# Performance work log

Measured on AMD Instinct MI355X. Metric: run time of the kernel, lower is better.

## Reference

```python
import jax, jax.numpy as jnp
import numpy as np

N_NODES = 50000
N_EDGES = 600000
F_IN, HID, N_CLS = 128, 128, 40
NEG_SLOPE = 0.2


def _gat_conv(x, src, dst, W, a_src, a_dst, b, num_nodes):
    # x: [N, Fin] -> h: [N, H]  (heads=1 PyG GATConv)
    h = x @ W
    s_src = h @ a_src  # [N]
    s_dst = h @ a_dst  # [N]
    e = jax.nn.leaky_relu(s_src[src] + s_dst[dst], NEG_SLOPE)  # [E]
    # numerically-stable softmax over incoming edges per destination node
    m = jax.ops.segment_max(e, dst, num_segments=num_nodes)  # [N]
    ex = jnp.exp(e - m[dst])
    denom = jax.ops.segment_sum(ex, dst, num_segments=num_nodes)  # [N]
    alpha = ex / denom[dst]  # [E]
    out = jax.ops.segment_sum(alpha[:, None] * h[src], dst, num_segments=num_nodes)
    return out + b


def setup_inputs() -> dict:
    key = jax.random.key(0)
    ks = jax.random.split(key, 10)
    x = jax.random.normal(ks[0], (N_NODES, F_IN), dtype=jnp.float32)
    edge_index = jax.random.randint(ks[1], (2, N_EDGES), 0, N_NODES, dtype=jnp.int64)
    sd = lambda fin: 1.0 / np.sqrt(fin)
    return {
        "x": x,
        "edge_index": edge_index,
        "W1": jax.random.normal(ks[2], (F_IN, HID), dtype=jnp.float32) * sd(F_IN),
        "a1_src": jax.random.normal(ks[3], (HID,), dtype=jnp.float32) * sd(HID),
        "a1_dst": jax.random.normal(ks[4], (HID,), dtype=jnp.float32) * sd(HID),
        "b1": jnp.zeros((HID,), dtype=jnp.float32),
        "W2": jax.random.normal(ks[5], (HID, HID), dtype=jnp.float32) * sd(HID),
        "a2_src": jax.random.normal(ks[6], (HID,), dtype=jnp.float32) * sd(HID),
        "a2_dst": jax.random.normal(ks[7], (HID,), dtype=jnp.float32) * sd(HID),
        "b2": jnp.zeros((HID,), dtype=jnp.float32),
        "Wl": jax.random.normal(ks[8], (HID, N_CLS), dtype=jnp.float32) * sd(HID),
        "bl": jnp.zeros((N_CLS,), dtype=jnp.float32),
    }


def reference(x, edge_index, W1, a1_src, a1_dst, b1, W2, a2_src, a2_dst, b2, Wl, bl):
    n = x.shape[0]
    # PyG GATConv adds self loops by default
    loops = jnp.arange(n, dtype=edge_index.dtype)
    src = jnp.concatenate([edge_index[0], loops])
    dst = jnp.concatenate([edge_index[1], loops])
    h = jax.nn.relu(_gat_conv(x, src, dst, W1, a1_src, a1_dst, b1, n))
    # F.dropout(training=self.training): eval mode -> identity
    h = _gat_conv(h, src, dst, W2, a2_src, a2_dst, b2, n)
    logits = jax.nn.log_softmax(h @ Wl + bl, axis=1)
    return (logits, edge_index)
```

## Files before the change

### kernel.cpp

```cpp
#include <hip/hip_runtime.h>
#include <hip/hip_bf16.h>
#include <math.h>

#define N_NODES 50000
#define N_EDGES 600000
#define TOT_E   (N_EDGES + N_NODES)
#define FDIM    128
#define HROW    64
#define NCLS    40
#define SCAN_B  1024

typedef __attribute__((ext_vector_type(4))) float  f32x4;
typedef __attribute__((ext_vector_type(8))) __bf16 bf16x8;
union FragU { uint32_t u[4]; bf16x8 v; };

__device__ inline float bf16_lo(uint32_t u) { return __uint_as_float(u << 16); }
__device__ inline float bf16_hi(uint32_t u) { return __uint_as_float(u & 0xffff0000u); }
__device__ inline uint32_t bf16_pack(float a, float b) {
    uint32_t ua = __float_as_uint(a), ub = __float_as_uint(b);
    uint32_t ra = (ua + 0x7fffu + ((ua >> 16) & 1u)) >> 16;
    uint32_t rb = (ub + 0x7fffu + ((ub >> 16) & 1u)) >> 16;
    return ra | (rb << 16);
}

#define PACK_BLOCKS 12500
__global__ __launch_bounds__(256) void setup_kernel(
        const float* __restrict__ x, uint32_t* __restrict__ Xp,
        const float* __restrict__ W1, const float* __restrict__ W2,
        uint32_t* __restrict__ wf1, uint32_t* __restrict__ wf2) {
    int b = blockIdx.x;
    if (b < PACK_BLOCKS) {
        int i = b * 256 + threadIdx.x;
        float2 v = ((const float2*)x)[i];
        Xp[i] = bf16_pack(v.x, v.y);
        return;
    }
    int t = (b - PACK_BLOCKS) * 256 + threadIdx.x;
    if (t >= 4096) return;
    const float* W = (t < 2048) ? W1 : W2;
    uint32_t*   wf = (t < 2048) ? wf1 : wf2;
    int q = t & 2047;
    int lane = q & 63, nt = (q >> 6) & 7, kt = q >> 9;
    int n = nt * 16 + (lane & 15), g = lane >> 4;
    uint32_t frag[4];
    #pragma unroll
    for (int d = 0; d < 4; d++) {
        int kb = kt * 32 + 4 * g + (d & 1) * 2 + (d >> 1) * 16;
        frag[d] = bf16_pack(W[kb * FDIM + n], W[(kb + 1) * FDIM + n]);
    }
    ((uint4*)wf)[(kt * 8 + nt) * 64 + lane] = *(uint4*)frag;
}

__global__ void hist_kernel(const int* __restrict__ ei, int* __restrict__ counts) {
    int i = blockIdx.x * blockDim.x + threadIdx.x;
    if (i >= N_EDGES / 4) return;
    int4 d = ((const int4*)(ei + N_EDGES))[i];
    atomicAdd(&counts[d.x], 1);
    atomicAdd(&counts[d.y], 1);
    atomicAdd(&counts[d.z], 1);
    atomicAdd(&counts[d.w], 1);
}

__global__ void scan1_kernel(const int* __restrict__ counts, int* __restrict__ excl,
                             int* __restrict__ bsums, int n) {
    __shared__ int ws[16];
    int gid = blockIdx.x * SCAN_B + threadIdx.x;
    int wv = threadIdx.x >> 6, lane = threadIdx.x & 63;
    int v = (gid < n) ? (counts[gid] + 1) : 0;
    int incl = v;
    #pragma unroll
    for (int off = 1; off < 64; off <<= 1) {
        int t = __shfl_up(incl, off, 64);
        if (lane >= off) incl += t;
    }
    if (lane == 63) ws[wv] = incl;
    __syncthreads();
    int woff = 0;
    for (int i = 0; i < wv; i++) woff += ws[i];
    if (gid < n) excl[gid] = woff + incl - v;
    if (threadIdx.x == SCAN_B - 1) bsums[blockIdx.x] = woff + incl;
}

__global__ void scan3_kernel(int* __restrict__ rowptr, const int* __restrict__ bsums,
                             int* __restrict__ cursor, int n, int total) {
    __shared__ int base_s;
    if (threadIdx.x < 64) {
        int v = (threadIdx.x < (int)blockIdx.x) ? bsums[threadIdx.x] : 0;
        #pragma unroll
        for (int off = 32; off > 0; off >>= 1) v += __shfl_down(v, off, 64);
        if (threadIdx.x == 0) base_s = v;
    }
    __syncthreads();
    int base = base_s;
    int gid = blockIdx.x * SCAN_B + threadIdx.x;
    if (gid < n) {
        int v = rowptr[gid] + base;
        rowptr[gid] = v;
        cursor[gid] = v;
    }
    if (gid == 0) rowptr[n] = total;
}

#define SCAT_T ((N_EDGES / 4) + N_NODES)
__global__ void scatter_kernel(const int* __restrict__ ei, int* __restrict__ cursor,
                               int* __restrict__ adj) {
    int i = blockIdx.x * blockDim.x + threadIdx.x;
    if (i >= SCAT_T) return;
    if (i < N_EDGES / 4) {
        int4 s4 = ((const int4*)ei)[i];
        int4 d4 = ((const int4*)(ei + N_EDGES))[i];
        adj[atomicAdd(&cursor[d4.x], 1)] = s4.x;
        adj[atomicAdd(&cursor[d4.y], 1)] = s4.y;
        adj[atomicAdd(&cursor[d4.z], 1)] = s4.z;
        adj[atomicAdd(&cursor[d4.w], 1)] = s4.w;
    } else {
        int nd = i - N_EDGES / 4;
        adj[atomicAdd(&cursor[nd], 1)] = nd;
    }
}

__global__ __launch_bounds__(256) void mfma_gemm(
        const uint32_t* __restrict__ Xp, const uint32_t* __restrict__ wf,
        const float* __restrict__ a_s, const float* __restrict__ a_d,
        uint32_t* __restrict__ H, float* __restrict__ ssrc, float* __restrict__ sdst) {
    int lane = threadIdx.x & 63, wv = threadIdx.x >> 6;
    int row0 = blockIdx.x * 64 + wv * 16;
    if (row0 >= N_NODES) return;
    int r = lane & 15, g = lane >> 4;

    const uint32_t* xrow = Xp + (size_t)(row0 + r) * HROW + 2 * g;
    FragU af[4];
    #pragma unroll
    for (int kt = 0; kt < 4; kt++) {
        uint2 lo = *(const uint2*)(xrow + kt * 16);
        uint2 hi = *(const uint2*)(xrow + kt * 16 + 8);
        af[kt].u[0] = lo.x; af[kt].u[1] = lo.y;
        af[kt].u[2] = hi.x; af[kt].u[3] = hi.y;
    }

    f32x4 acc[8] = {};
    #pragma unroll
    for (int kt = 0; kt < 4; kt++) {
        #pragma unroll
        for (int nt = 0; nt < 8; nt++) {
            FragU bfr;
            *(uint4*)bfr.u = ((const uint4*)wf)[(kt * 8 + nt) * 64 + lane];
            acc[nt] = __builtin_amdgcn_mfma_f32_16x16x32_bf16(af[kt].v, bfr.v, acc[nt], 0, 0, 0);
        }
    }

    float av_s[8], av_d[8];
    #pragma unroll
    for (int nt = 0; nt < 8; nt++) { av_s[nt] = a_s[16 * nt + r]; av_d[nt] = a_d[16 * nt + r]; }
    #pragma unroll
    for (int j = 0; j < 4; j++) {
        float ps = 0.f, pd = 0.f;
        #pragma unroll
        for (int nt = 0; nt < 8; nt++) { ps += acc[nt][j] * av_s[nt]; pd += acc[nt][j] * av_d[nt]; }
        #pragma unroll
        for (int off = 1; off < 16; off <<= 1) {
            ps += __shfl_xor(ps, off, 64);
            pd += __shfl_xor(pd, off, 64);
        }
        if (r == 0) { ssrc[row0 + 4 * g + j] = ps; sdst[row0 + 4 * g + j] = pd; }
    }

    #pragma unroll
    for (int nt = 0; nt < 8; nt++) {
        #pragma unroll
        for (int j = 0; j < 4; j++) {
            float v0 = acc[nt][j];
            float v1 = __shfl_xor(v0, 1, 64);
            if (!(r & 1)) {
                uint32_t p = bf16_pack(v0, v1);
                H[(size_t)(row0 + 4 * g + j) * HROW + nt * 8 + (r >> 1)] = p;
            }
        }
    }
}

__global__ __launch_bounds__(128) void gat_aggregate(
        const uint32_t* __restrict__ h, const float* __restrict__ ssrc,
        const float* __restrict__ sdst, const int* __restrict__ rowptr,
        const int* __restrict__ adj, const float* __restrict__ bias,
        uint32_t* __restrict__ out, int do_relu) {
    int wv = threadIdx.x >> 6, lane = threadIdx.x & 63;
    int sub = lane >> 4, l16 = lane & 15;
    int n = blockIdx.x * 2 + wv;
    __shared__ __align__(16) float wbuf[2][64];
    __shared__ __align__(16) int   sbuf[2][64];

    int beg = rowptr[n], deg = rowptr[n + 1] - beg;
    float sd = sdst[n];
    const uint4* h4 = (const uint4*)h;

    float acc[8] = {};
    float dsum = 0.f;

    for (int base = 0; base < deg; base += 64) {
        int c = min(64, deg - base);
        if (lane < c) {
            int s = adj[beg + base + lane];
            float e = ssrc[s] + sd;
            e = (e >= 0.f) ? e : 0.2f * e;
            float w = __expf(e);
            wbuf[wv][lane] = w;
            sbuf[wv][lane] = s;
            dsum += w;
        }
        asm volatile("s_waitcnt lgkmcnt(0)" ::: "memory");

        int j = 0;
        for (; j + 16 <= c; j += 16) {
            float4 w4 = *(const float4*)&wbuf[wv][j + 4 * sub];
            int4   s4 = *(const int4*)&sbuf[wv][j + 4 * sub];
            uint4 u0 = h4[(size_t)s4.x * 16 + l16];
            uint4 u1 = h4[(size_t)s4.y * 16 + l16];
            uint4 u2 = h4[(size_t)s4.z * 16 + l16];
            uint4 u3 = h4[(size_t)s4.w * 16 + l16];
            acc[0] += w4.x * bf16_lo(u0.x) + w4.y * bf16_lo(u1.x) + w4.z * bf16_lo(u2.x) + w4.w * bf16_lo(u3.x);
            acc[1] += w4.x * bf16_hi(u0.x) + w4.y * bf16_hi(u1.x) + w4.z * bf16_hi(u2.x) + w4.w * bf16_hi(u3.x);
            acc[2] += w4.x * bf16_lo(u0.y) + w4.y * bf16_lo(u1.y) + w4.z * bf16_lo(u2.y) + w4.w * bf16_lo(u3.y);
            acc[3] += w4.x * bf16_hi(u0.y) + w4.y * bf16_hi(u1.y) + w4.z * bf16_hi(u2.y) + w4.w * bf16_hi(u3.y);
            acc[4] += w4.x * bf16_lo(u0.z) + w4.y * bf16_lo(u1.z) + w4.z * bf16_lo(u2.z) + w4.w * bf16_lo(u3.z);
            acc[5] += w4.x * bf16_hi(u0.z) + w4.y * bf16_hi(u1.z) + w4.z * bf16_hi(u2.z) + w4.w * bf16_hi(u3.z);
            acc[6] += w4.x * bf16_lo(u0.w) + w4.y * bf16_lo(u1.w) + w4.z * bf16_lo(u2.w) + w4.w * bf16_lo(u3.w);
            acc[7] += w4.x * bf16_hi(u0.w) + w4.y * bf16_hi(u1.w) + w4.z * bf16_hi(u2.w) + w4.w * bf16_hi(u3.w);
        }
        for (; j < c; j += 4) {
            int e = j + sub;
            if (e < c) {
                float w = wbuf[wv][e];
                int   s = sbuf[wv][e];
                uint4 u = h4[(size_t)s * 16 + l16];
                acc[0] += w * bf16_lo(u.x); acc[1] += w * bf16_hi(u.x);
                acc[2] += w * bf16_lo(u.y); acc[3] += w * bf16_hi(u.y);
                acc[4] += w * bf16_lo(u.z); acc[5] += w * bf16_hi(u.z);
                acc[6] += w * bf16_lo(u.w); acc[7] += w * bf16_hi(u.w);
            }
        }
        asm volatile("" ::: "memory");
    }

    #pragma unroll
    for (int k = 0; k < 8; k++) {
        acc[k] += __shfl_xor(acc[k], 16, 64);
        acc[k] += __shfl_xor(acc[k], 32, 64);
    }
    #pragma unroll
    for (int off = 32; off > 0; off >>= 1) dsum += __shfl_xor(dsum, off, 64);

    if (sub == 0) {
        float inv = 1.f / dsum;
        float4 b0 = *(const float4*)&bias[l16 * 8];
        float4 b1 = *(const float4*)&bias[l16 * 8 + 4];
        float v0 = acc[0] * inv + b0.x, v1 = acc[1] * inv + b0.y;
        float v2 = acc[2] * inv + b0.z, v3 = acc[3] * inv + b0.w;
        float v4 = acc[4] * inv + b1.x, v5 = acc[5] * inv + b1.y;
        float v6 = acc[6] * inv + b1.z, v7 = acc[7] * inv + b1.w;
        if (do_relu) {
            v0 = fmaxf(v0, 0.f); v1 = fmaxf(v1, 0.f); v2 = fmaxf(v2, 0.f); v3 = fmaxf(v3, 0.f);
            v4 = fmaxf(v4, 0.f); v5 = fmaxf(v5, 0.f); v6 = fmaxf(v6, 0.f); v7 = fmaxf(v7, 0.f);
        }
        uint4 o;
        o.x = bf16_pack(v0, v1); o.y = bf16_pack(v2, v3);
        o.z = bf16_pack(v4, v5); o.w = bf16_pack(v6, v7);
        ((uint4*)out)[(size_t)n * 16 + l16] = o;
    }
}

#define CLS_BLOCKS  (N_NODES / 16)
#define EDGE_ITEMS  ((2 * N_EDGES) / 4)
#define EDGE_BLOCKS ((EDGE_ITEMS + 127) / 128)
__global__ __launch_bounds__(128) void classifier_edge_kernel(
        const uint32_t* __restrict__ H, const float* __restrict__ Wl,
        const float* __restrict__ bl, const int* __restrict__ ei,
        float* __restrict__ out, float* __restrict__ eout) {
    if (blockIdx.x >= CLS_BLOCKS) {
        int i = (blockIdx.x - CLS_BLOCKS) * 128 + threadIdx.x;
        if (i < EDGE_ITEMS) {
            int4 v = ((const int4*)ei)[i];
            ((float4*)eout)[i] = make_float4((float)v.x, (float)v.y, (float)v.z, (float)v.w);
        }
        return;
    }
    __shared__ float xs[16][FDIM];
    int tid  = threadIdx.x;
    int row0 = blockIdx.x * 16;
    const uint32_t* Hp = H + (size_t)row0 * HROW;
    #pragma unroll
    for (int i = 0; i < 8; i++) {
        int idx = tid + 128 * i;
        uint32_t u = Hp[idx];
        int r = idx >> 6, cc = idx & 63;
        xs[r][2 * cc]     = bf16_lo(u);
        xs[r][2 * cc + 1] = bf16_hi(u);
    }
    __syncthreads();

    int c = tid & 63, hw = tid >> 6;
    float acc[8];
    float blc = (c < NCLS) ? bl[c] : 0.f;
    #pragma unroll
    for (int r = 0; r < 8; r++) acc[r] = blc;

    #pragma unroll 2
    for (int k = 0; k < FDIM; k += 4) {
        float w0 = 0.f, w1 = 0.f, w2 = 0.f, w3 = 0.f;
        if (c < NCLS) {
            w0 = Wl[(k + 0) * NCLS + c]; w1 = Wl[(k + 1) * NCLS + c];
            w2 = Wl[(k + 2) * NCLS + c]; w3 = Wl[(k + 3) * NCLS + c];
        }
        #pragma unroll
        for (int r = 0; r < 8; r++) {
            float4 xv = *(const float4*)&xs[hw * 8 + r][k];
            acc[r] += xv.x * w0 + xv.y * w1 + xv.z * w2 + xv.w * w3;
        }
    }
    #pragma unroll
    for (int r = 0; r < 8; r++) {
        float v = (c < NCLS) ? acc[r] : -INFINITY;
        float mx = v;
        #pragma unroll
        for (int off = 32; off > 0; off >>= 1) mx = fmaxf(mx, __shfl_xor(mx, off, 64));
        float ex = (c < NCLS) ? expf(v - mx) : 0.f;
        #pragma unroll
        for (int off = 32; off > 0; off >>= 1) ex += __shfl_xor(ex, off, 64);
        float ls = logf(ex);
        if (c < NCLS) out[(size_t)(row0 + hw * 8 + r) * NCLS + c] = v - mx - ls;
    }
}

extern "C" void kernel_launch(void* const* d_in, const int* in_sizes, int n_in,
                              void* d_out, int out_size, void* d_ws, size_t ws_size,
                              hipStream_t stream) {
    const float* x   = (const float*)d_in[0];
    const int*   ei  = (const int*)d_in[1];
    const float* W1  = (const float*)d_in[2];
    const float* a1s = (const float*)d_in[3];
    const float* a1d = (const float*)d_in[4];
    const float* b1  = (const float*)d_in[5];
    const float* W2  = (const float*)d_in[6];
    const float* a2s = (const float*)d_in[7];
    const float* a2d = (const float*)d_in[8];
    const float* b2  = (const float*)d_in[9];
    const float* Wl  = (const float*)d_in[10];
    const float* bl  = (const float*)d_in[11];
    float* out = (float*)d_out;

    char* ws = (char*)d_ws;
    size_t off = 0;
    auto alloc = [&](size_t bytes) {
        void* p = ws + off;
        off = (off + bytes + 255) & ~(size_t)255;
        return p;
    };
    int*      row_ptr = (int*)alloc((N_NODES + 1) * sizeof(int));
    int*      cursor  = (int*)alloc(N_NODES * sizeof(int));
    int*      counts  = (int*)alloc(N_NODES * sizeof(int));
    int*      bsums   = (int*)alloc(64 * sizeof(int));
    int*      adj     = (int*)alloc(TOT_E * sizeof(int));
    uint32_t* Xp      = (uint32_t*)alloc((size_t)N_NODES * HROW * sizeof(uint32_t));
    uint32_t* hA      = (uint32_t*)alloc((size_t)N_NODES * HROW * sizeof(uint32_t));
    uint32_t* hB      = (uint32_t*)alloc((size_t)N_NODES * HROW * sizeof(uint32_t));
    float*    ssrc    = (float*)alloc(N_NODES * sizeof(float));
    float*    sdst    = (float*)alloc(N_NODES * sizeof(float));
    uint32_t* wf1     = (uint32_t*)alloc(2048 * 4 * sizeof(uint32_t));
    uint32_t* wf2     = (uint32_t*)alloc(2048 * 4 * sizeof(uint32_t));
    uint32_t* hC      = Xp;

    hipMemsetAsync(counts, 0, N_NODES * sizeof(int), stream);
    hipLaunchKernelGGL(setup_kernel, dim3(PACK_BLOCKS + 16), dim3(256), 0, stream,
                       x, Xp, W1, W2, wf1, wf2);

    hipLaunchKernelGGL(hist_kernel, dim3((N_EDGES / 4 + 255) / 256), dim3(256), 0, stream, ei, counts);
    int nscan = (N_NODES + SCAN_B - 1) / SCAN_B;
    hipLaunchKernelGGL(scan1_kernel, dim3(nscan), dim3(SCAN_B), 0, stream, counts, row_ptr, bsums, N_NODES);
    hipLaunchKernelGGL(scan3_kernel, dim3(nscan), dim3(SCAN_B), 0, stream, row_ptr, bsums, cursor, N_NODES, TOT_E);
    hipLaunchKernelGGL(scatter_kernel, dim3((SCAT_T + 255) / 256), dim3(256), 0, stream, ei, cursor, adj);

    hipLaunchKernelGGL(mfma_gemm, dim3((N_NODES + 63) / 64), dim3(256), 0, stream,
                       Xp, wf1, a1s, a1d, hA, ssrc, sdst);
    hipLaunchKernelGGL(gat_aggregate, dim3(N_NODES / 2), dim3(128), 0, stream,
                       hA, ssrc, sdst, row_ptr, adj, b1, hB, 1);

    hipLaunchKernelGGL(mfma_gemm, dim3((N_NODES + 63) / 64), dim3(256), 0, stream,
                       hB, wf2, a2s, a2d, hA, ssrc, sdst);
    hipLaunchKernelGGL(gat_aggregate, dim3(N_NODES / 2), dim3(128), 0, stream,
                       hA, ssrc, sdst, row_ptr, adj, b2, hC, 0);

    hipLaunchKernelGGL(classifier_edge_kernel, dim3(CLS_BLOCKS + EDGE_BLOCKS), dim3(128), 0, stream,
                       hC, Wl, bl, ei, out, out + (size_t)N_NODES * NCLS);
}
```

Baseline: 291.8 us.

## Fuse GAT pipeline into fewer kernels: agg+GEMM, agg+classifier, scatter+GEMM

```diff
diff --git a/kernel.cpp b/kernel.cpp
--- a/kernel.cpp
+++ b/kernel.cpp
@@ -23,180 +23,11 @@
     return ra | (rb << 16);
 }
 
-#define PACK_BLOCKS 12500
-__global__ __launch_bounds__(256) void setup_kernel(
-        const float* __restrict__ x, uint32_t* __restrict__ Xp,
-        const float* __restrict__ W1, const float* __restrict__ W2,
-        uint32_t* __restrict__ wf1, uint32_t* __restrict__ wf2) {
-    int b = blockIdx.x;
-    if (b < PACK_BLOCKS) {
-        int i = b * 256 + threadIdx.x;
-        float2 v = ((const float2*)x)[i];
-        Xp[i] = bf16_pack(v.x, v.y);
-        return;
-    }
-    int t = (b - PACK_BLOCKS) * 256 + threadIdx.x;
-    if (t >= 4096) return;
-    const float* W = (t < 2048) ? W1 : W2;
-    uint32_t*   wf = (t < 2048) ? wf1 : wf2;
-    int q = t & 2047;
-    int lane = q & 63, nt = (q >> 6) & 7, kt = q >> 9;
-    int n = nt * 16 + (lane & 15), g = lane >> 4;
-    uint32_t frag[4];
-    #pragma unroll
-    for (int d = 0; d < 4; d++) {
-        int kb = kt * 32 + 4 * g + (d & 1) * 2 + (d >> 1) * 16;
-        frag[d] = bf16_pack(W[kb * FDIM + n], W[(kb + 1) * FDIM + n]);
-    }
-    ((uint4*)wf)[(kt * 8 + nt) * 64 + lane] = *(uint4*)frag;
-}
-
-__global__ void hist_kernel(const int* __restrict__ ei, int* __restrict__ counts) {
-    int i = blockIdx.x * blockDim.x + threadIdx.x;
-    if (i >= N_EDGES / 4) return;
-    int4 d = ((const int4*)(ei + N_EDGES))[i];
-    atomicAdd(&counts[d.x], 1);
-    atomicAdd(&counts[d.y], 1);
-    atomicAdd(&counts[d.z], 1);
-    atomicAdd(&counts[d.w], 1);
-}
-
-__global__ void scan1_kernel(const int* __restrict__ counts, int* __restrict__ excl,
-                             int* __restrict__ bsums, int n) {
-    __shared__ int ws[16];
-    int gid = blockIdx.x * SCAN_B + threadIdx.x;
-    int wv = threadIdx.x >> 6, lane = threadIdx.x & 63;
-    int v = (gid < n) ? (counts[gid] + 1) : 0;
-    int incl = v;
-    #pragma unroll
-    for (int off = 1; off < 64; off <<= 1) {
-        int t = __shfl_up(incl, off, 64);
-        if (lane >= off) incl += t;
-    }
-    if (lane == 63) ws[wv] = incl;
-    __syncthreads();
-    int woff = 0;
-    for (int i = 0; i < wv; i++) woff += ws[i];
-    if (gid < n) excl[gid] = woff + incl - v;
-    if (threadIdx.x == SCAN_B - 1) bsums[blockIdx.x] = woff + incl;
-}
-
-__global__ void scan3_kernel(int* __restrict__ rowptr, const int* __restrict__ bsums,
-                             int* __restrict__ cursor, int n, int total) {
-    __shared__ int base_s;
-    if (threadIdx.x < 64) {
-        int v = (threadIdx.x < (int)blockIdx.x) ? bsums[threadIdx.x] : 0;
-        #pragma unroll
-        for (int off = 32; off > 0; off >>= 1) v += __shfl_down(v, off, 64);
-        if (threadIdx.x == 0) base_s = v;
-    }
-    __syncthreads();
-    int base = base_s;
-    int gid = blockIdx.x * SCAN_B + threadIdx.x;
-    if (gid < n) {
-        int v = rowptr[gid] + base;
-        rowptr[gid] = v;
-        cursor[gid] = v;
-    }
-    if (gid == 0) rowptr[n] = total;
-}
-
-#define SCAT_T ((N_EDGES / 4) + N_NODES)
-__global__ void scatter_kernel(const int* __restrict__ ei, int* __restrict__ cursor,
-                               int* __restrict__ adj) {
-    int i = blockIdx.x * blockDim.x + threadIdx.x;
-    if (i >= SCAT_T) return;
-    if (i < N_EDGES / 4) {
-        int4 s4 = ((const int4*)ei)[i];
-        int4 d4 = ((const int4*)(ei + N_EDGES))[i];
-        adj[atomicAdd(&cursor[d4.x], 1)] = s4.x;
-        adj[atomicAdd(&cursor[d4.y], 1)] = s4.y;
-        adj[atomicAdd(&cursor[d4.z], 1)] = s4.z;
-        adj[atomicAdd(&cursor[d4.w], 1)] = s4.w;
-    } else {
-        int nd = i - N_EDGES / 4;
-        adj[atomicAdd(&cursor[nd], 1)] = nd;
-    }
-}
-
-__global__ __launch_bounds__(256) void mfma_gemm(
-        const uint32_t* __restrict__ Xp, const uint32_t* __restrict__ wf,
-        const float* __restrict__ a_s, const float* __restrict__ a_d,
-        uint32_t* __restrict__ H, float* __restrict__ ssrc, float* __restrict__ sdst) {
-    int lane = threadIdx.x & 63, wv = threadIdx.x >> 6;
-    int row0 = blockIdx.x * 64 + wv * 16;
-    if (row0 >= N_NODES) return;
-    int r = lane & 15, g = lane >> 4;
-
-    const uint32_t* xrow = Xp + (size_t)(row0 + r) * HROW + 2 * g;
-    FragU af[4];
-    #pragma unroll
-    for (int kt = 0; kt < 4; kt++) {
-        uint2 lo = *(const uint2*)(xrow + kt * 16);
-        uint2 hi = *(const uint2*)(xrow + kt * 16 + 8);
-        af[kt].u[0] = lo.x; af[kt].u[1] = lo.y;
-        af[kt].u[2] = hi.x; af[kt].u[3] = hi.y;
-    }
-
-    f32x4 acc[8] = {};
-    #pragma unroll
-    for (int kt = 0; kt < 4; kt++) {
-        #pragma unroll
-        for (int nt = 0; nt < 8; nt++) {
-            FragU bfr;
-            *(uint4*)bfr.u = ((const uint4*)wf)[(kt * 8 + nt) * 64 + lane];
-            acc[nt] = __builtin_amdgcn_mfma_f32_16x16x32_bf16(af[kt].v, bfr.v, acc[nt], 0, 0, 0);
-        }
-    }
-
-    float av_s[8], av_d[8];
-    #pragma unroll
-    for (int nt = 0; nt < 8; nt++) { av_s[nt] = a_s[16 * nt + r]; av_d[nt] = a_d[16 * nt + r]; }
-    #pragma unroll
-    for (int j = 0; j < 4; j++) {
-        float ps = 0.f, pd = 0.f;
-        #pragma unroll
-        for (int nt = 0; nt < 8; nt++) { ps += acc[nt][j] * av_s[nt]; pd += acc[nt][j] * av_d[nt]; }
-        #pragma unroll
-        for (int off = 1; off < 16; off <<= 1) {
-            ps += __shfl_xor(ps, off, 64);
-            pd += __shfl_xor(pd, off, 64);
-        }
-        if (r == 0) { ssrc[row0 + 4 * g + j] = ps; sdst[row0 + 4 * g + j] = pd; }
-    }
-
-    #pragma unroll
-    for (int nt = 0; nt < 8; nt++) {
-        #pragma unroll
-        for (int j = 0; j < 4; j++) {
-            float v0 = acc[nt][j];
-            float v1 = __shfl_xor(v0, 1, 64);
-            if (!(r & 1)) {
-                uint32_t p = bf16_pack(v0, v1);
-                H[(size_t)(row0 + 4 * g + j) * HROW + nt * 8 + (r >> 1)] = p;
-            }
-        }
-    }
-}
-
-__global__ __launch_bounds__(128) void gat_aggregate(
-        const uint32_t* __restrict__ h, const float* __restrict__ ssrc,
-        const float* __restrict__ sdst, const int* __restrict__ rowptr,
-        const int* __restrict__ adj, const float* __restrict__ bias,
-        uint32_t* __restrict__ out, int do_relu) {
-    int wv = threadIdx.x >> 6, lane = threadIdx.x & 63;
-    int sub = lane >> 4, l16 = lane & 15;
-    int n = blockIdx.x * 2 + wv;
-    __shared__ __align__(16) float wbuf[2][64];
-    __shared__ __align__(16) int   sbuf[2][64];
-
-    int beg = rowptr[n], deg = rowptr[n + 1] - beg;
-    float sd = sdst[n];
-    const uint4* h4 = (const uint4*)h;
-
-    float acc[8] = {};
-    float dsum = 0.f;
-
+__device__ __forceinline__ void wave_agg_loop(
+        const uint4* __restrict__ h4, const float* __restrict__ ssrc,
+        const int* __restrict__ adj, float sd, int beg, int deg,
+        float* wb, int* sb, int lane, int sub, int l16,
+        float acc[8], float& dsum) {
     for (int base = 0; base < deg; base += 64) {
         int c = min(64, deg - base);
         if (lane < c) {
@@ -204,16 +35,16 @@
             float e = ssrc[s] + sd;
             e = (e >= 0.f) ? e : 0.2f * e;
             float w = __expf(e);
-            wbuf[wv][lane] = w;
-            sbuf[wv][lane] = s;
+            wb[lane] = w;
+            sb[lane] = s;
             dsum += w;
         }
         asm volatile("s_waitcnt lgkmcnt(0)" ::: "memory");
 
         int j = 0;
         for (; j + 16 <= c; j += 16) {
-            float4 w4 = *(const float4*)&wbuf[wv][j + 4 * sub];
-            int4   s4 = *(const int4*)&sbuf[wv][j + 4 * sub];
+            float4 w4 = *(const float4*)&wb[j + 4 * sub];
+            int4   s4 = *(const int4*)&sb[j + 4 * sub];
             uint4 u0 = h4[(size_t)s4.x * 16 + l16];
             uint4 u1 = h4[(size_t)s4.y * 16 + l16];
             uint4 u2 = h4[(size_t)s4.z * 16 + l16];
@@ -230,8 +61,8 @@
         for (; j < c; j += 4) {
             int e = j + sub;
             if (e < c) {
-                float w = wbuf[wv][e];
-                int   s = sbuf[wv][e];
+                float w = wb[e];
+                int   s = sb[e];
                 uint4 u = h4[(size_t)s * 16 + l16];
                 acc[0] += w * bf16_lo(u.x); acc[1] += w * bf16_hi(u.x);
                 acc[2] += w * bf16_lo(u.y); acc[3] += w * bf16_hi(u.y);
@@ -241,7 +72,6 @@
         }
         asm volatile("" ::: "memory");
     }
-
     #pragma unroll
     for (int k = 0; k < 8; k++) {
         acc[k] += __shfl_xor(acc[k], 16, 64);
@@ -249,60 +79,312 @@
     }
     #pragma unroll
     for (int off = 32; off > 0; off >>= 1) dsum += __shfl_xor(dsum, off, 64);
-
-    if (sub == 0) {
-        float inv = 1.f / dsum;
-        float4 b0 = *(const float4*)&bias[l16 * 8];
-        float4 b1 = *(const float4*)&bias[l16 * 8 + 4];
-        float v0 = acc[0] * inv + b0.x, v1 = acc[1] * inv + b0.y;
-        float v2 = acc[2] * inv + b0.z, v3 = acc[3] * inv + b0.w;
-        float v4 = acc[4] * inv + b1.x, v5 = acc[5] * inv + b1.y;
-        float v6 = acc[6] * inv + b1.z, v7 = acc[7] * inv + b1.w;
-        if (do_relu) {
-            v0 = fmaxf(v0, 0.f); v1 = fmaxf(v1, 0.f); v2 = fmaxf(v2, 0.f); v3 = fmaxf(v3, 0.f);
-            v4 = fmaxf(v4, 0.f); v5 = fmaxf(v5, 0.f); v6 = fmaxf(v6, 0.f); v7 = fmaxf(v7, 0.f);
-        }
-        uint4 o;
-        o.x = bf16_pack(v0, v1); o.y = bf16_pack(v2, v3);
-        o.z = bf16_pack(v4, v5); o.w = bf16_pack(v6, v7);
-        ((uint4*)out)[(size_t)n * 16 + l16] = o;
-    }
-}
-
-#define CLS_BLOCKS  (N_NODES / 16)
+}
+
+#define PACK_BLOCKS  12500
+#define WFRAG_BLOCKS 16
+#define HIST_BLOCKS  ((N_EDGES / 4 + 255) / 256)
+__global__ __launch_bounds__(256) void k1_setup_hist(
+        const float* __restrict__ x, uint32_t* __restrict__ Xp,
+        const float* __restrict__ W1, const float* __restrict__ W2,
+        uint32_t* __restrict__ wf1, uint32_t* __restrict__ wf2,
+        const int* __restrict__ ei, int* __restrict__ counts) {
+    int b = blockIdx.x;
+    if (b < PACK_BLOCKS) {
+        int i = b * 256 + threadIdx.x;
+        float2 v = ((const float2*)x)[i];
+        Xp[i] = bf16_pack(v.x, v.y);
+        return;
+    }
+    if (b < PACK_BLOCKS + WFRAG_BLOCKS) {
+        int t = (b - PACK_BLOCKS) * 256 + threadIdx.x;
+        if (t >= 4096) return;
+        const float* W = (t < 2048) ? W1 : W2;
+        uint32_t*   wf = (t < 2048) ? wf1 : wf2;
+        int q = t & 2047;
+        int lane = q & 63, nt = (q >> 6) & 7, kt = q >> 9;
+        int n = nt * 16 + (lane & 15), g = lane >> 4;
+        uint32_t frag[4];
+        #pragma unroll
+        for (int d = 0; d < 4; d++) {
+            int kb = kt * 32 + 4 * g + (d & 1) * 2 + (d >> 1) * 16;
+            frag[d] = bf16_pack(W[kb * FDIM + n], W[(kb + 1) * FDIM + n]);
+        }
+        ((uint4*)wf)[(kt * 8 + nt) * 64 + lane] = *(uint4*)frag;
+        return;
+    }
+    int i = (b - PACK_BLOCKS - WFRAG_BLOCKS) * 256 + threadIdx.x;
+    if (i >= N_EDGES / 4) return;
+    int4 d = ((const int4*)(ei + N_EDGES))[i];
+    atomicAdd(&counts[d.x], 1);
+    atomicAdd(&counts[d.y], 1);
+    atomicAdd(&counts[d.z], 1);
+    atomicAdd(&counts[d.w], 1);
+}
+
+__global__ void scan1_kernel(const int* __restrict__ counts, int* __restrict__ excl,
+                             int* __restrict__ bsums, int n) {
+    __shared__ int ws[16];
+    int gid = blockIdx.x * SCAN_B + threadIdx.x;
+    int wv = threadIdx.x >> 6, lane = threadIdx.x & 63;
+    int v = (gid < n) ? (counts[gid] + 1) : 0;
+    int incl = v;
+    #pragma unroll
+    for (int off = 1; off < 64; off <<= 1) {
+        int t = __shfl_up(incl, off, 64);
+        if (lane >= off) incl += t;
+    }
+    if (lane == 63) ws[wv] = incl;
+    __syncthreads();
+    int woff = 0;
+    for (int i = 0; i < wv; i++) woff += ws[i];
+    if (gid < n) excl[gid] = woff + incl - v;
+    if (threadIdx.x == SCAN_B - 1) bsums[blockIdx.x] = woff + incl;
+}
+
+__global__ void scan3_kernel(int* __restrict__ rowptr, const int* __restrict__ bsums,
+                             int* __restrict__ cursor, int n, int total) {
+    __shared__ int base_s;
+    if (threadIdx.x < 64) {
+        int v = (threadIdx.x < (int)blockIdx.x) ? bsums[threadIdx.x] : 0;
+        #pragma unroll
+        for (int off = 32; off > 0; off >>= 1) v += __shfl_down(v, off, 64);
+        if (threadIdx.x == 0) base_s = v;
+    }
+    __syncthreads();
+    int base = base_s;
+    int gid = blockIdx.x * SCAN_B + threadIdx.x;
+    if (gid < n) {
+        int v = rowptr[gid] + base;
+        rowptr[gid] = v;
+        cursor[gid] = v;
+    }
+    if (gid == 0) rowptr[n] = total;
+}
+
+#define SCAT_T      ((N_EDGES / 4) + N_NODES)
+#define SCAT_BLOCKS ((SCAT_T + 255) / 256)
+#define GEMM_BLOCKS ((N_NODES + 63) / 64)
 #define EDGE_ITEMS  ((2 * N_EDGES) / 4)
-#define EDGE_BLOCKS ((EDGE_ITEMS + 127) / 128)
-__global__ __launch_bounds__(128) void classifier_edge_kernel(
-        const uint32_t* __restrict__ H, const float* __restrict__ Wl,
-        const float* __restrict__ bl, const int* __restrict__ ei,
-        float* __restrict__ out, float* __restrict__ eout) {
-    if (blockIdx.x >= CLS_BLOCKS) {
-        int i = (blockIdx.x - CLS_BLOCKS) * 128 + threadIdx.x;
-        if (i < EDGE_ITEMS) {
-            int4 v = ((const int4*)ei)[i];
-            ((float4*)eout)[i] = make_float4((float)v.x, (float)v.y, (float)v.z, (float)v.w);
+#define EDGE_BLOCKS ((EDGE_ITEMS + 255) / 256)
+__global__ __launch_bounds__(256) void k4_scatter_gemm_edge(
+        const int* __restrict__ ei, int* __restrict__ cursor, int* __restrict__ adj,
+        const uint32_t* __restrict__ Xp, const uint32_t* __restrict__ wf,
+        const float* __restrict__ a_s, const float* __restrict__ a_d,
+        uint32_t* __restrict__ H, float* __restrict__ ssrc, float* __restrict__ sdst,
+        float* __restrict__ eout) {
+    int b = blockIdx.x;
+    if (b < SCAT_BLOCKS) {
+        int i = b * 256 + threadIdx.x;
+        if (i >= SCAT_T) return;
+        if (i < N_EDGES / 4) {
+            int4 s4 = ((const int4*)ei)[i];
+            int4 d4 = ((const int4*)(ei + N_EDGES))[i];
+            adj[atomicAdd(&cursor[d4.x], 1)] = s4.x;
+            adj[atomicAdd(&cursor[d4.y], 1)] = s4.y;
+            adj[atomicAdd(&cursor[d4.z], 1)] = s4.z;
+            adj[atomicAdd(&cursor[d4.w], 1)] = s4.w;
+        } else {
+            int nd = i - N_EDGES / 4;
+            adj[atomicAdd(&cursor[nd], 1)] = nd;
         }
         return;
     }
+    if (b < SCAT_BLOCKS + GEMM_BLOCKS) {
+        int lane = threadIdx.x & 63, wv = threadIdx.x >> 6;
+        int row0 = (b - SCAT_BLOCKS) * 64 + wv * 16;
+        if (row0 >= N_NODES) return;
+        int r = lane & 15, g = lane >> 4;
+
+        const uint32_t* xrow = Xp + (size_t)(row0 + r) * HROW + 2 * g;
+        FragU af[4];
+        #pragma unroll
+        for (int kt = 0; kt < 4; kt++) {
+            uint2 lo = *(const uint2*)(xrow + kt * 16);
+            uint2 hi = *(const uint2*)(xrow + kt * 16 + 8);
+            af[kt].u[0] = lo.x; af[kt].u[1] = lo.y;
+            af[kt].u[2] = hi.x; af[kt].u[3] = hi.y;
+        }
+        f32x4 acc[8] = {};
+        #pragma unroll
+        for (int kt = 0; kt < 4; kt++) {
+            #pragma unroll
+            for (int nt = 0; nt < 8; nt++) {
+                FragU bfr;
+                *(uint4*)bfr.u = ((const uint4*)wf)[(kt * 8 + nt) * 64 + lane];
+                acc[nt] = __builtin_amdgcn_mfma_f32_16x16x32_bf16(af[kt].v, bfr.v, acc[nt], 0, 0, 0);
+            }
+        }
+        float av_s[8], av_d[8];
+        #pragma unroll
+        for (int nt = 0; nt < 8; nt++) { av_s[nt] = a_s[16 * nt + r]; av_d[nt] = a_d[16 * nt + r]; }
+        #pragma unroll
+        for (int j = 0; j < 4; j++) {
+            float ps = 0.f, pd = 0.f;
+            #pragma unroll
+            for (int nt = 0; nt < 8; nt++) { ps += acc[nt][j] * av_s[nt]; pd += acc[nt][j] * av_d[nt]; }
+            #pragma unroll
+            for (int off = 1; off < 16; off <<= 1) {
+                ps += __shfl_xor(ps, off, 64);
+                pd += __shfl_xor(pd, off, 64);
+            }
+            if (r == 0) { ssrc[row0 + 4 * g + j] = ps; sdst[row0 + 4 * g + j] = pd; }
+        }
+        #pragma unroll
+        for (int nt = 0; nt < 8; nt++) {
+            #pragma unroll
+            for (int j = 0; j < 4; j++) {
+                float v0 = acc[nt][j];
+                float v1 = __shfl_xor(v0, 1, 64);
+                if (!(r & 1))
+                    H[(size_t)(row0 + 4 * g + j) * HROW + nt * 8 + (r >> 1)] = bf16_pack(v0, v1);
+            }
+        }
+        return;
+    }
+    int i = (b - SCAT_BLOCKS - GEMM_BLOCKS) * 256 + threadIdx.x;
+    if (i < EDGE_ITEMS) {
+        int4 v = ((const int4*)ei)[i];
+        ((float4*)eout)[i] = make_float4((float)v.x, (float)v.y, (float)v.z, (float)v.w);
+    }
+}
+
+__global__ __launch_bounds__(256) void k5_agg_gemm(
+        const uint32_t* __restrict__ h, const float* __restrict__ ssrc,
+        const float* __restrict__ sdst, const int* __restrict__ rowptr,
+        const int* __restrict__ adj, const float* __restrict__ bias,
+        const uint32_t* __restrict__ wf, const float* __restrict__ a_s,
+        const float* __restrict__ a_d, uint32_t* __restrict__ Hout,
+        float* __restrict__ ssrc2, float* __restrict__ sdst2) {
+    int tid = threadIdx.x;
+    int wv = tid >> 6, lane = tid & 63;
+    int sub = lane >> 4, l16 = lane & 15;
+    int row0 = blockIdx.x * 16;
+    __shared__ __align__(16) float    wbuf[4][64];
+    __shared__ __align__(16) int      sbuf[4][64];
+    __shared__ __align__(16) uint32_t rowbuf[16][68];
+    __shared__ float scS[4][16], scD[4][16];
+    const uint4* h4 = (const uint4*)h;
+
+    for (int i = 0; i < 4; i++) {
+        int row = wv * 4 + i;
+        int n = row0 + row;
+        int beg = rowptr[n], deg = rowptr[n + 1] - beg;
+        float acc[8] = {};
+        float dsum = 0.f;
+        wave_agg_loop(h4, ssrc, adj, sdst[n], beg, deg, wbuf[wv], sbuf[wv],
+                      lane, sub, l16, acc, dsum);
+        if (sub == 0) {
+            float inv = 1.f / dsum;
+            float4 b0 = *(const float4*)&bias[l16 * 8];
+            float4 b1 = *(const float4*)&bias[l16 * 8 + 4];
+            float v0 = fmaxf(acc[0] * inv + b0.x, 0.f), v1 = fmaxf(acc[1] * inv + b0.y, 0.f);
+            float v2 = fmaxf(acc[2] * inv + b0.z, 0.f), v3 = fmaxf(acc[3] * inv + b0.w, 0.f);
+            float v4 = fmaxf(acc[4] * inv + b1.x, 0.f), v5 = fmaxf(acc[5] * inv + b1.y, 0.f);
+            float v6 = fmaxf(acc[6] * inv + b1.z, 0.f), v7 = fmaxf(acc[7] * inv + b1.w, 0.f);
+            uint4 o;
+            o.x = bf16_pack(v0, v1); o.y = bf16_pack(v2, v3);
+            o.z = bf16_pack(v4, v5); o.w = bf16_pack(v6, v7);
+            *(uint4*)&rowbuf[row][l16 * 4] = o;
+        }
+    }
+    __syncthreads();
+
+    int r = lane & 15, g = lane >> 4;
+    FragU af[4];
+    #pragma unroll
+    for (int kt = 0; kt < 4; kt++) {
+        uint2 lo = *(const uint2*)&rowbuf[r][kt * 16 + 2 * g];
+        uint2 hi = *(const uint2*)&rowbuf[r][kt * 16 + 2 * g + 8];
+        af[kt].u[0] = lo.x; af[kt].u[1] = lo.y;
+        af[kt].u[2] = hi.x; af[kt].u[3] = hi.y;
+    }
+    f32x4 acc2[2] = {};
+    #pragma unroll
+    for (int kt = 0; kt < 4; kt++) {
+        #pragma unroll
+        for (int t = 0; t < 2; t++) {
+            int nt = 2 * wv + t;
+            FragU bfr;
+            *(uint4*)bfr.u = ((const uint4*)wf)[(kt * 8 + nt) * 64 + lane];
+            acc2[t] = __builtin_amdgcn_mfma_f32_16x16x32_bf16(af[kt].v, bfr.v, acc2[t], 0, 0, 0);
+        }
+    }
+    float as0 = a_s[16 * (2 * wv) + r], as1 = a_s[16 * (2 * wv + 1) + r];
+    float ad0 = a_d[16 * (2 * wv) + r], ad1 = a_d[16 * (2 * wv + 1) + r];
+    #pragma unroll
+    for (int j = 0; j < 4; j++) {
+        float ps = acc2[0][j] * as0 + acc2[1][j] * as1;
+        float pd = acc2[0][j] * ad0 + acc2[1][j] * ad1;
+        #pragma unroll
+        for (int off = 1; off < 16; off <<= 1) {
+            ps += __shfl_xor(ps, off, 64);
+            pd += __shfl_xor(pd, off, 64);
+        }
+        if (r == 0) { scS[wv][4 * g + j] = ps; scD[wv][4 * g + j] = pd; }
+    }
+    #pragma unroll
+    for (int t = 0; t < 2; t++) {
+        #pragma unroll
+        for (int j = 0; j < 4; j++) {
+            float v0 = acc2[t][j];
+            float v1 = __shfl_xor(v0, 1, 64);
+            if (!(r & 1))
+                Hout[(size_t)(row0 + 4 * g + j) * HROW + (2 * wv + t) * 8 + (r >> 1)] = bf16_pack(v0, v1);
+        }
+    }
+    __syncthreads();
+    if (tid < 16)
+        ssrc2[row0 + tid] = scS[0][tid] + scS[1][tid] + scS[2][tid] + scS[3][tid];
+    else if (tid < 32) {
+        int q = tid - 16;
+        sdst2[row0 + q] = scD[0][q] + scD[1][q] + scD[2][q] + scD[3][q];
+    }
+}
+
+__global__ __launch_bounds__(256) void k6_agg_cls(
+        const uint32_t* __restrict__ h, const float* __restrict__ ssrc,
+        const float* __restrict__ sdst, const int* __restrict__ rowptr,
+        const int* __restrict__ adj, const float* __restrict__ bias,
+        const float* __restrict__ Wl, const float* __restrict__ bl,
+        float* __restrict__ out) {
+    int tid = threadIdx.x;
+    int wv = tid >> 6, lane = tid & 63;
+    int sub = lane >> 4, l16 = lane & 15;
+    int row0 = blockIdx.x * 16;
+    __shared__ __align__(16) float wbuf[4][64];
+    __shared__ __align__(16) int   sbuf[4][64];
     __shared__ float xs[16][FDIM];
-    int tid  = threadIdx.x;
-    int row0 = blockIdx.x * 16;
-    const uint32_t* Hp = H + (size_t)row0 * HROW;
-    #pragma unroll
-    for (int i = 0; i < 8; i++) {
-        int idx = tid + 128 * i;
-        uint32_t u = Hp[idx];
-        int r = idx >> 6, cc = idx & 63;
-        xs[r][2 * cc]     = bf16_lo(u);
-        xs[r][2 * cc + 1] = bf16_hi(u);
+    const uint4* h4 = (const uint4*)h;
+
+    for (int i = 0; i < 4; i++) {
+        int row = wv * 4 + i;
+        int n = row0 + row;
+        int beg = rowptr[n], deg = rowptr[n + 1] - beg;
+        float acc[8] = {};
+        float dsum = 0.f;
+        wave_agg_loop(h4, ssrc, adj, sdst[n], beg, deg, wbuf[wv], sbuf[wv],
+                      lane, sub, l16, acc, dsum);
+        if (sub == 0) {
+            float inv = 1.f / dsum;
+            float4 b0 = *(const float4*)&bias[l16 * 8];
+            float4 b1 = *(const float4*)&bias[l16 * 8 + 4];
+            float4 p0, p1;
+            p0.x = acc[0] * inv + b0.x; p0.y = acc[1] * inv + b0.y;
+            p0.z = acc[2] * inv + b0.z; p0.w = acc[3] * inv + b0.w;
+            p1.x = acc[4] * inv + b1.x; p1.y = acc[5] * inv + b1.y;
+            p1.z = acc[6] * inv + b1.z; p1.w = acc[7] * inv + b1.w;
+            *(float4*)&xs[row][l16 * 8]     = p0;
+            *(float4*)&xs[row][l16 * 8 + 4] = p1;
+        }
     }
     __syncthreads();
 
     int c = tid & 63, hw = tid >> 6;
-    float acc[8];
+    float acc[4];
     float blc = (c < NCLS) ? bl[c] : 0.f;
     #pragma unroll
-    for (int r = 0; r < 8; r++) acc[r] = blc;
+    for (int r = 0; r < 4; r++) acc[r] = blc;
 
     #pragma unroll 2
     for (int k = 0; k < FDIM; k += 4) {
@@ -312,13 +394,13 @@
             w2 = Wl[(k + 2) * NCLS + c]; w3 = Wl[(k + 3) * NCLS + c];
         }
         #pragma unroll
-        for (int r = 0; r < 8; r++) {
-            float4 xv = *(const float4*)&xs[hw * 8 + r][k];
+        for (int r = 0; r < 4; r++) {
+            float4 xv = *(const float4*)&xs[hw * 4 + r][k];
             acc[r] += xv.x * w0 + xv.y * w1 + xv.z * w2 + xv.w * w3;
         }
     }
     #pragma unroll
-    for (int r = 0; r < 8; r++) {
+    for (int r = 0; r < 4; r++) {
         float v = (c < NCLS) ? acc[r] : -INFINITY;
         float mx = v;
         #pragma unroll
@@ -327,7 +409,7 @@
         #pragma unroll
         for (int off = 32; off > 0; off >>= 1) ex += __shfl_xor(ex, off, 64);
         float ls = logf(ex);
-        if (c < NCLS) out[(size_t)(row0 + hw * 8 + r) * NCLS + c] = v - mx - ls;
+        if (c < NCLS) out[(size_t)(row0 + hw * 4 + r) * NCLS + c] = v - mx - ls;
     }
 }
 
@@ -365,30 +447,27 @@
     uint32_t* hB      = (uint32_t*)alloc((size_t)N_NODES * HROW * sizeof(uint32_t));
     float*    ssrc    = (float*)alloc(N_NODES * sizeof(float));
     float*    sdst    = (float*)alloc(N_NODES * sizeof(float));
+    float*    ssrc2   = (float*)alloc(N_NODES * sizeof(float));
+    float*    sdst2   = (float*)alloc(N_NODES * sizeof(float));
     uint32_t* wf1     = (uint32_t*)alloc(2048 * 4 * sizeof(uint32_t));
     uint32_t* wf2     = (uint32_t*)alloc(2048 * 4 * sizeof(uint32_t));
-    uint32_t* hC      = Xp;
 
     hipMemsetAsync(counts, 0, N_NODES * sizeof(int), stream);
-    hipLaunchKernelGGL(setup_kernel, dim3(PACK_BLOCKS + 16), dim3(256), 0, stream,
-                       x, Xp, W1, W2, wf1, wf2);
-
-    hipLaunchKernelGGL(hist_kernel, dim3((N_EDGES / 4 + 255) / 256), dim3(256), 0, stream, ei, counts);
+
+    hipLaunchKernelGGL(k1_setup_hist, dim3(PACK_BLOCKS + WFRAG_BLOCKS + HIST_BLOCKS), dim3(256),
+                       0, stream, x, Xp, W1, W2, wf1, wf2, ei, counts);
+
     int nscan = (N_NODES + SCAN_B - 1) / SCAN_B;
     hipLaunchKernelGGL(scan1_kernel, dim3(nscan), dim3(SCAN_B), 0, stream, counts, row_ptr, bsums, N_NODES);
     hipLaunchKernelGGL(scan3_kernel, dim3(nscan), dim3(SCAN_B), 0, stream, row_ptr, bsums, cursor, N_NODES, TOT_E);
-    hipLaunchKernelGGL(scatter_kernel, dim3((SCAT_T + 255) / 256), dim3(256), 0, stream, ei, cursor, adj);
-
-    hipLaunchKernelGGL(mfma_gemm, dim3((N_NODES + 63) / 64), dim3(256), 0, stream,
-                       Xp, wf1, a1s, a1d, hA, ssrc, sdst);
-    hipLaunchKernelGGL(gat_aggregate, dim3(N_NODES / 2), dim3(128), 0, stream,
-                       hA, ssrc, sdst, row_ptr, adj, b1, hB, 1);
-
-    hipLaunchKernelGGL(mfma_gemm, dim3((N_NODES + 63) / 64), dim3(256), 0, stream,
-                       hB, wf2, a2s, a2d, hA, ssrc, sdst);
-    hipLaunchKernelGGL(gat_aggregate, dim3(N_NODES / 2), dim3(128), 0, stream,
-                       hA, ssrc, sdst, row_ptr, adj, b2, hC, 0);
-
-    hipLaunchKernelGGL(classifier_edge_kernel, dim3(CLS_BLOCKS + EDGE_BLOCKS), dim3(128), 0, stream,
-                       hC, Wl, bl, ei, out, out + (size_t)N_NODES * NCLS);
-}
+
+    hipLaunchKernelGGL(k4_scatter_gemm_edge, dim3(SCAT_BLOCKS + GEMM_BLOCKS + EDGE_BLOCKS), dim3(256),
+                       0, stream, ei, cursor, adj, Xp, wf1, a1s, a1d, hA, ssrc, sdst,
+                       out + (size_t)N_NODES * NCLS);
+
+    hipLaunchKernelGGL(k5_agg_gemm, dim3(N_NODES / 16), dim3(256), 0, stream,
+                       hA, ssrc, sdst, row_ptr, adj, b1, wf2, a2s, a2d, hB, ssrc2, sdst2);
+
+    hipLaunchKernelGGL(k6_agg_cls, dim3(N_NODES / 16), dim3(256), 0, stream,
+                       hB, ssrc2, sdst2, row_ptr, adj, b2, Wl, bl, out);
+}
```

Result: faster. 285.7 us (-2.1%).
